# Optimization experiments

Measured on AMD Instinct MI355X. Metric: run time of the kernel, lower is better.

Reference implementation:

```python
import jax, jax.numpy as jnp
import numpy as np

N, E, L, H, D, HID = 32768, 262144, 4, 8, 64, 512
IN_DIM, OUT_DIM, EDIM, MAX_SP = 386, 384, 32, 4


def setup_inputs() -> dict:
    key = jax.random.key(0)
    k = jax.random.split(key, 16)
    s = 0.02
    d = {}
    d["embeddings"] = jax.random.normal(k[0], (N, IN_DIM), jnp.float32)
    d["edge_index"] = jax.random.randint(k[1], (2, E), 0, N)
    d["edge_attr_ids"] = jax.random.randint(k[2], (E,), 0, MAX_SP)
    d["Win"] = jax.random.normal(k[3], (IN_DIM, HID)) * s
    d["bin_"] = jnp.zeros((HID,))
    d["Etab"] = jax.random.normal(k[4], (MAX_SP, EDIM)) * s
    d["Wq"] = jax.random.normal(k[5], (L, HID, HID)) * s
    d["bq"] = jnp.zeros((L, HID))
    d["Wk"] = jax.random.normal(k[6], (L, HID, HID)) * s
    d["bk"] = jnp.zeros((L, HID))
    d["Wv"] = jax.random.normal(k[7], (L, HID, HID)) * s
    d["bv"] = jnp.zeros((L, HID))
    d["We"] = jax.random.normal(k[8], (L, EDIM, HID)) * s
    d["be"] = jnp.zeros((L, HID))
    d["Ws"] = jax.random.normal(k[9], (L, HID, HID)) * s
    d["bs"] = jnp.zeros((L, HID))
    d["Wbeta"] = jax.random.normal(k[10], (L, 3 * HID, 1)) * s
    d["bbeta"] = jnp.zeros((L, 1))
    d["ln_g"] = jnp.ones((L, HID))
    d["ln_b"] = jnp.zeros((L, HID))
    d["Wout"] = jax.random.normal(k[11], (HID, OUT_DIM)) * s
    d["bout"] = jnp.zeros((OUT_DIM,))
    return d


def _ln(x, g, b):
    mu = x.mean(-1, keepdims=True)
    var = ((x - mu) ** 2).mean(-1, keepdims=True)
    return (x - mu) * jax.lax.rsqrt(var + 1e-5) * g + b


def _fwd(embeddings, edge_index, edge_attr_ids, Win, bin_, Etab, Wq, bq, Wk, bk,
         Wv, bv, We, be, Ws, bs, Wbeta, bbeta, ln_g, ln_b, Wout, bout):
    src, dst = edge_index[0], edge_index[1]  # messages flow src -> dst (PyG convention)
    h = embeddings @ Win + bin_              # [N, HID]
    e = Etab[edge_attr_ids]                  # [E, EDIM]
    scale = 1.0 / np.sqrt(D).astype(np.float32)
    for l in range(L):
        q = (h @ Wq[l] + bq[l]).reshape(N, H, D)
        kk = (h @ Wk[l] + bk[l]).reshape(N, H, D)
        v = (h @ Wv[l] + bv[l]).reshape(N, H, D)
        ee = (e @ We[l] + be[l]).reshape(E, H, D)
        kj = kk[src] + ee                    # [E, H, D]
        vj = v[src] + ee                     # [E, H, D]
        alpha = jnp.einsum('ehd,ehd->eh', q[dst], kj) * scale  # [E, H]
        # segment softmax over incoming edges of each target node
        amax = jax.lax.stop_gradient(jax.ops.segment_max(alpha, dst, num_segments=N))
        ex = jnp.exp(alpha - amax[dst])
        denom = jax.ops.segment_sum(ex, dst, num_segments=N)
        a = ex / denom[dst]                  # [E, H] (dropout in eval mode -> identity)
        out = jax.ops.segment_sum(a[..., None] * vj, dst, num_segments=N).reshape(N, HID)
        # beta-gated skip connection (PyG TransformerConv beta=True)
        xr = h @ Ws[l] + bs[l]
        beta = jax.nn.sigmoid(jnp.concatenate([out, xr, out - xr], axis=-1) @ Wbeta[l] + bbeta[l])
        out = beta * xr + (1.0 - beta) * out
        h = _ln(h + out, ln_g[l], ln_b[l])
    return h @ Wout + bout


def reference(embeddings, edge_index, edge_attr_ids, Win, bin_, Etab, Wq, bq, Wk,
              bk, Wv, bv, We, be, Ws, bs, Wbeta, bbeta, ln_g, ln_b, Wout, bout):
    return _fwd(embeddings, edge_index, edge_attr_ids, Win, bin_, Etab, Wq, bq,
                Wk, bk, Wv, bv, We, be, Ws, bs, Wbeta, bbeta, ln_g, ln_b, Wout, bout)
```

## Files before the change

### kernel.cpp

```cpp
#include <hip/hip_runtime.h>
#include <math.h>

#define NN      32768
#define EE_N    262144
#define LL      4
#define HID     512
#define IN_DIM  386
#define KP_IN   416
#define OUT_DIM 384
#define EDIM    32
#define MAX_SP  4

typedef __attribute__((ext_vector_type(8))) __bf16 bf16x8;
typedef __attribute__((ext_vector_type(4))) float  f32x4;

__device__ __forceinline__ unsigned short f2bf(float f) {
    unsigned int u = __float_as_uint(f);
    unsigned int r = (u + 0x7FFFu + ((u >> 16) & 1u)) >> 16;
    return (unsigned short)r;
}
__device__ __forceinline__ void unpack2(unsigned int w, float& lo, float& hi) {
    lo = __uint_as_float(w << 16);
    hi = __uint_as_float(w & 0xFFFF0000u);
}

template <int OUT_MODE>
__global__ __launch_bounds__(256) void gemm_mfma(
    const unsigned short* __restrict__ A,
    const unsigned short* __restrict__ Bt,
    const float* __restrict__ bias,
    void* __restrict__ C0, void* __restrict__ C1,
    int M, int Kp, int N)
{
    __shared__ unsigned short As[128 * 32];
    __shared__ unsigned short Bs[128 * 32];

    const int t    = threadIdx.x;
    const int lane = t & 63, wid = t >> 6;
    const int wr   = wid >> 1, wc = wid & 1;
    const int row0 = blockIdx.y * 128;
    const int col0 = blockIdx.x * 128;

    f32x4 acc[4][4] = {};

    const int srow  = lane >> 2;
    const int sslot = lane & 3;
    const int kq    = lane >> 4;
    const int l15   = lane & 15;

    for (int kt = 0; kt < Kp; kt += 32) {
#pragma unroll
        for (int i = 0; i < 2; ++i) {
            const int rbase = wid * 32 + i * 16;
            {
                const int r    = rbase + srow;
                const int koff = sslot ^ ((r >> 1) & 3);
                const unsigned short* ga = &A[(size_t)(row0 + r) * Kp + kt + koff * 8];
                __builtin_amdgcn_global_load_lds(
                    (const __attribute__((address_space(1))) unsigned int*)ga,
                    (__attribute__((address_space(3))) unsigned int*)&As[rbase * 32],
                    16, 0, 0);
            }
            {
                const int c    = rbase + srow;
                const int koff = sslot ^ ((c >> 1) & 3);
                const unsigned short* gb = &Bt[(size_t)(col0 + c) * Kp + kt + koff * 8];
                __builtin_amdgcn_global_load_lds(
                    (const __attribute__((address_space(1))) unsigned int*)gb,
                    (__attribute__((address_space(3))) unsigned int*)&Bs[rbase * 32],
                    16, 0, 0);
            }
        }
        __syncthreads();

        bf16x8 af[4], bf[4];
#pragma unroll
        for (int mi = 0; mi < 4; ++mi) {
            const int r    = wr * 64 + mi * 16 + l15;
            const int slot = kq ^ ((r >> 1) & 3);
            af[mi] = *reinterpret_cast<const bf16x8*>(&As[r * 32 + slot * 8]);
        }
#pragma unroll
        for (int ni = 0; ni < 4; ++ni) {
            const int c    = wc * 64 + ni * 16 + l15;
            const int slot = kq ^ ((c >> 1) & 3);
            bf[ni] = *reinterpret_cast<const bf16x8*>(&Bs[c * 32 + slot * 8]);
        }
#pragma unroll
        for (int mi = 0; mi < 4; ++mi)
#pragma unroll
            for (int ni = 0; ni < 4; ++ni)
                acc[mi][ni] = __builtin_amdgcn_mfma_f32_16x16x32_bf16(
                    af[mi], bf[ni], acc[mi][ni], 0, 0, 0);
        __syncthreads();
    }

    const int cb = col0 + wc * 64;
    const int rb = row0 + wr * 64;
    float bv[4];
#pragma unroll
    for (int ni = 0; ni < 4; ++ni) bv[ni] = bias[cb + ni * 16 + l15];

#pragma unroll
    for (int mi = 0; mi < 4; ++mi) {
#pragma unroll
        for (int ni = 0; ni < 4; ++ni) {
            const int col = cb + ni * 16 + l15;
#pragma unroll
            for (int r = 0; r < 4; ++r) {
                const int row = rb + mi * 16 + kq * 4 + r;
                const float oval = acc[mi][ni][r] + bv[ni];
                if (OUT_MODE == 0) {
                    ((float*)C0)[(size_t)row * N + col] = oval;
                } else if (OUT_MODE == 1) {
                    ((unsigned short*)C0)[(size_t)row * N + col] = f2bf(oval);
                } else {
                    ((float*)C0)[(size_t)row * N + col] = oval;
                    ((unsigned short*)C1)[(size_t)row * N + col] = f2bf(oval);
                }
            }
        }
    }
}

__global__ __launch_bounds__(256) void convert_wt(
    const float* __restrict__ W, unsigned short* __restrict__ Wt,
    int K, int N, int Kp)
{
    __shared__ float tile[32][33];
    const int tx = threadIdx.x, ty = threadIdx.y;
    const int kb = blockIdx.y * 32, nb = blockIdx.x * 32;
#pragma unroll
    for (int i = 0; i < 32; i += 8) {
        const int k = kb + ty + i, n = nb + tx;
        tile[ty + i][tx] = (k < K && n < N) ? W[(size_t)k * N + n] : 0.f;
    }
    __syncthreads();
#pragma unroll
    for (int i = 0; i < 32; i += 8) {
        const int n = nb + ty + i, k = kb + tx;
        if (n < N && k < Kp)
            Wt[(size_t)n * Kp + k] = f2bf(tile[tx][ty + i]);
    }
}

__global__ __launch_bounds__(256) void convert_emb(
    const float* __restrict__ emb, unsigned short* __restrict__ ebf)
{
    const int n = blockIdx.x;
    for (int k = threadIdx.x; k < KP_IN; k += 256)
        ebf[(size_t)n * KP_IN + k] =
            (k < IN_DIM) ? f2bf(emb[(size_t)n * IN_DIM + k]) : (unsigned short)0;
}

__global__ void ee_kernel(const float* __restrict__ Etab,
                          const float* __restrict__ We,
                          const float* __restrict__ be,
                          float* __restrict__ ee)
{
    int j = threadIdx.x;
    if (j < HID) {
        for (int a = 0; a < MAX_SP; ++a) {
            float s = be[j];
            for (int kk = 0; kk < EDIM; ++kk)
                s = fmaf(Etab[a * EDIM + kk], We[kk * HID + j], s);
            ee[a * HID + j] = s;
        }
    }
}

__global__ void hist_kernel(const int* __restrict__ dst, int* __restrict__ deg)
{
    int e = blockIdx.x * blockDim.x + threadIdx.x;
    if (e < EE_N) atomicAdd(&deg[dst[e]], 1);
}

__global__ __launch_bounds__(1024) void scan_kernel(
    const int* __restrict__ deg, int* __restrict__ row_ptr, int* __restrict__ cursor)
{
    __shared__ int sdata[1024];
    const int t = threadIdx.x;
    const int base = t * 32;
    int s = 0;
    for (int i = 0; i < 32; ++i) s += deg[base + i];
    sdata[t] = s;
    __syncthreads();
    for (int off = 1; off < 1024; off <<= 1) {
        int val = (t >= off) ? sdata[t - off] : 0;
        __syncthreads();
        sdata[t] += val;
        __syncthreads();
    }
    int run = sdata[t] - s;
    for (int i = 0; i < 32; ++i) {
        row_ptr[base + i] = run;
        cursor[base + i]  = run;
        run += deg[base + i];
    }
    if (t == 1023) row_ptr[NN] = run;
}

__global__ void scatter_kernel(const int* __restrict__ src, const int* __restrict__ dst,
                               const int* __restrict__ aid, int* __restrict__ cursor,
                               int* __restrict__ csr_src, int* __restrict__ csr_aid)
{
    int e = blockIdx.x * blockDim.x + threadIdx.x;
    if (e < EE_N) {
        int d = dst[e];
        int pos = atomicAdd(&cursor[d], 1);
        csr_src[pos] = src[e];
        csr_aid[pos] = aid[e];
    }
}

__global__ __launch_bounds__(256) void attn_kernel(
    const unsigned short* __restrict__ q, const unsigned short* __restrict__ k,
    const unsigned short* __restrict__ v, const float* __restrict__ ee,
    const int* __restrict__ row_ptr, const int* __restrict__ csr_src,
    const int* __restrict__ csr_aid, unsigned short* __restrict__ out)
{
    __shared__ float ees[MAX_SP * HID];
    const int t = threadIdx.x;
    for (int i = t; i < MAX_SP * HID; i += 256) ees[i] = ee[i];
    __syncthreads();

    const int wave = t >> 6, lane = t & 63;
    const int node = blockIdx.x * 4 + wave;
    const int off  = lane << 3;

    float qa[8];
    {
        uint4 qv = *reinterpret_cast<const uint4*>(&q[(size_t)node * HID + off]);
        unpack2(qv.x, qa[0], qa[1]); unpack2(qv.y, qa[2], qa[3]);
        unpack2(qv.z, qa[4], qa[5]); unpack2(qv.w, qa[6], qa[7]);
    }

    float m = -INFINITY, denom = 0.f;
    float acc[8] = {0.f, 0.f, 0.f, 0.f, 0.f, 0.f, 0.f, 0.f};

    const int beg = row_ptr[node], end = row_ptr[node + 1];
    for (int i = beg; i < end; ++i) {
        const int s   = csr_src[i];
        const int aid = csr_aid[i];
        const float* ep = &ees[aid * HID + off];

        float kj[8];
        {
            uint4 kv = *reinterpret_cast<const uint4*>(&k[(size_t)s * HID + off]);
            unpack2(kv.x, kj[0], kj[1]); unpack2(kv.y, kj[2], kj[3]);
            unpack2(kv.z, kj[4], kj[5]); unpack2(kv.w, kj[6], kj[7]);
        }
        float partial = 0.f;
#pragma unroll
        for (int j = 0; j < 8; ++j) partial = fmaf(qa[j], kj[j] + ep[j], partial);
        partial += __shfl_xor(partial, 1);
        partial += __shfl_xor(partial, 2);
        partial += __shfl_xor(partial, 4);
        const float alpha = partial * 0.125f;

        const float mnew = fmaxf(m, alpha);
        const float corr = expf(m - mnew);
        const float w    = expf(alpha - mnew);
        denom = denom * corr + w;

        float vj[8];
        {
            uint4 vv = *reinterpret_cast<const uint4*>(&v[(size_t)s * HID + off]);
            unpack2(vv.x, vj[0], vj[1]); unpack2(vv.y, vj[2], vj[3]);
            unpack2(vv.z, vj[4], vj[5]); unpack2(vv.w, vj[6], vj[7]);
        }
#pragma unroll
        for (int j = 0; j < 8; ++j) acc[j] = acc[j] * corr + w * (vj[j] + ep[j]);
        m = mnew;
    }

    const float inv = (denom > 0.f) ? (1.f / denom) : 0.f;
    union { unsigned short us[8]; uint4 v4; } pk;
#pragma unroll
    for (int j = 0; j < 8; ++j) pk.us[j] = f2bf(acc[j] * inv);
    *reinterpret_cast<uint4*>(&out[(size_t)node * HID + off]) = pk.v4;
}

__global__ __launch_bounds__(256) void blend_ln_kernel(
    float* __restrict__ h, unsigned short* __restrict__ hbf,
    const unsigned short* __restrict__ attn,
    const unsigned short* __restrict__ xr, const float* __restrict__ wbeta,
    const float* __restrict__ bbeta, const float* __restrict__ ln_g,
    const float* __restrict__ ln_b)
{
    const int t = threadIdx.x;
    const int wave = t >> 6, lane = t & 63;
    const int node = blockIdx.x * 4 + wave;
    const int off  = lane << 3;

    float o8[8], x8[8], h8[8];
    {
        uint4 a = *reinterpret_cast<const uint4*>(&attn[(size_t)node * HID + off]);
        unpack2(a.x, o8[0], o8[1]); unpack2(a.y, o8[2], o8[3]);
        unpack2(a.z, o8[4], o8[5]); unpack2(a.w, o8[6], o8[7]);
        uint4 b = *reinterpret_cast<const uint4*>(&xr[(size_t)node * HID + off]);
        unpack2(b.x, x8[0], x8[1]); unpack2(b.y, x8[2], x8[3]);
        unpack2(b.z, x8[4], x8[5]); unpack2(b.w, x8[6], x8[7]);
        float4 c0 = *reinterpret_cast<const float4*>(&h[(size_t)node * HID + off]);
        float4 c1 = *reinterpret_cast<const float4*>(&h[(size_t)node * HID + off + 4]);
        h8[0]=c0.x; h8[1]=c0.y; h8[2]=c0.z; h8[3]=c0.w; h8[4]=c1.x; h8[5]=c1.y; h8[6]=c1.z; h8[7]=c1.w;
    }

    float p = 0.f;
#pragma unroll
    for (int j = 0; j < 8; ++j) {
        float w1 = wbeta[off + j];
        float w2 = wbeta[HID + off + j];
        float w3 = wbeta[2 * HID + off + j];
        p = fmaf(o8[j], w1 + w3, p);
        p = fmaf(x8[j], w2 - w3, p);
    }
#pragma unroll
    for (int m = 1; m <= 32; m <<= 1) p += __shfl_xor(p, m);
    const float beta = 1.f / (1.f + expf(-(p + bbeta[0])));

    float y[8];
    float s = 0.f;
#pragma unroll
    for (int j = 0; j < 8; ++j) {
        y[j] = h8[j] + beta * x8[j] + (1.f - beta) * o8[j];
        s += y[j];
    }
#pragma unroll
    for (int m = 1; m <= 32; m <<= 1) s += __shfl_xor(s, m);
    const float mean = s * (1.f / HID);

    float vs = 0.f;
#pragma unroll
    for (int j = 0; j < 8; ++j) {
        float d = y[j] - mean;
        vs = fmaf(d, d, vs);
    }
#pragma unroll
    for (int m = 1; m <= 32; m <<= 1) vs += __shfl_xor(vs, m);
    const float rstd = rsqrtf(vs * (1.f / HID) + 1e-5f);

    float rr[8];
    union { unsigned short us[8]; uint4 v4; } pk;
#pragma unroll
    for (int j = 0; j < 8; ++j) {
        rr[j] = (y[j] - mean) * rstd * ln_g[off + j] + ln_b[off + j];
        pk.us[j] = f2bf(rr[j]);
    }
    float4 r0 = {rr[0], rr[1], rr[2], rr[3]};
    float4 r1 = {rr[4], rr[5], rr[6], rr[7]};
    *reinterpret_cast<float4*>(&h[(size_t)node * HID + off])     = r0;
    *reinterpret_cast<float4*>(&h[(size_t)node * HID + off + 4]) = r1;
    *reinterpret_cast<uint4*>(&hbf[(size_t)node * HID + off])    = pk.v4;
}

extern "C" void kernel_launch(void* const* d_in, const int* in_sizes, int n_in,
                              void* d_out, int out_size, void* d_ws, size_t ws_size,
                              hipStream_t stream)
{
    (void)in_sizes; (void)n_in; (void)out_size; (void)ws_size;
    const float* emb   = (const float*)d_in[0];
    const int*   eidx  = (const int*)d_in[1];
    const int*   aid   = (const int*)d_in[2];
    const float* Win   = (const float*)d_in[3];
    const float* bin_  = (const float*)d_in[4];
    const float* Etab  = (const float*)d_in[5];
    const float* Wq    = (const float*)d_in[6];
    const float* bq    = (const float*)d_in[7];
    const float* Wk    = (const float*)d_in[8];
    const float* bk    = (const float*)d_in[9];
    const float* Wv    = (const float*)d_in[10];
    const float* bv    = (const float*)d_in[11];
    const float* We    = (const float*)d_in[12];
    const float* be    = (const float*)d_in[13];
    const float* Ws    = (const float*)d_in[14];
    const float* bs    = (const float*)d_in[15];
    const float* Wbeta = (const float*)d_in[16];
    const float* bbeta = (const float*)d_in[17];
    const float* ln_g  = (const float*)d_in[18];
    const float* ln_b  = (const float*)d_in[19];
    const float* Wout  = (const float*)d_in[20];
    const float* bout  = (const float*)d_in[21];
    float* out = (float*)d_out;

    char* w = (char*)d_ws;
    float* h            = (float*)w;           w += (size_t)NN * HID * 4;
    unsigned short* q   = (unsigned short*)w;  w += (size_t)NN * HID * 2;
    unsigned short* k   = (unsigned short*)w;  w += (size_t)NN * HID * 2;
    unsigned short* v   = (unsigned short*)w;  w += (size_t)NN * HID * 2;
    unsigned short* hbf = (unsigned short*)w;  w += (size_t)NN * HID * 2;
    unsigned short* embbf = q;
    unsigned short* Winbf  = (unsigned short*)w; w += (size_t)HID * KP_IN * 2;
    unsigned short* Wlt    = (unsigned short*)w; w += (size_t)16 * HID * HID * 2;
    unsigned short* Woutbf = (unsigned short*)w; w += (size_t)OUT_DIM * HID * 2;
    float* ee    = (float*)w;  w += MAX_SP * HID * 4;
    int* row_ptr = (int*)w;    w += (NN + 4) * 4;
    int* cursor  = (int*)w;    w += NN * 4;
    int* deg     = (int*)w;    w += NN * 4;
    int* csr_src = (int*)w;    w += EE_N * 4;
    int* csr_aid = (int*)w;    w += EE_N * 4;

    const int* src = eidx;
    const int* dst = eidx + EE_N;

    hipMemsetAsync(deg, 0, NN * sizeof(int), stream);
    hist_kernel<<<EE_N / 256, 256, 0, stream>>>(dst, deg);
    scan_kernel<<<1, 1024, 0, stream>>>(deg, row_ptr, cursor);
    scatter_kernel<<<EE_N / 256, 256, 0, stream>>>(src, dst, aid, cursor, csr_src, csr_aid);

    dim3 tb(32, 8);
    convert_wt<<<dim3(HID / 32, KP_IN / 32), tb, 0, stream>>>(Win, Winbf, IN_DIM, HID, KP_IN);
    for (int l = 0; l < LL; ++l) {
        convert_wt<<<dim3(16, 16), tb, 0, stream>>>(Wq + (size_t)l * HID * HID, Wlt + (size_t)(l * 4 + 0) * HID * HID, HID, HID, HID);
        convert_wt<<<dim3(16, 16), tb, 0, stream>>>(Wk + (size_t)l * HID * HID, Wlt + (size_t)(l * 4 + 1) * HID * HID, HID, HID, HID);
        convert_wt<<<dim3(16, 16), tb, 0, stream>>>(Wv + (size_t)l * HID * HID, Wlt + (size_t)(l * 4 + 2) * HID * HID, HID, HID, HID);
        convert_wt<<<dim3(16, 16), tb, 0, stream>>>(Ws + (size_t)l * HID * HID, Wlt + (size_t)(l * 4 + 3) * HID * HID, HID, HID, HID);
    }
    convert_wt<<<dim3(OUT_DIM / 32, HID / 32), tb, 0, stream>>>(Wout, Woutbf, HID, OUT_DIM, HID);
    convert_emb<<<NN, 256, 0, stream>>>(emb, embbf);

    gemm_mfma<2><<<dim3(HID / 128, NN / 128), 256, 0, stream>>>(
        embbf, Winbf, bin_, h, hbf, NN, KP_IN, HID);

    for (int l = 0; l < LL; ++l) {
        ee_kernel<<<1, HID, 0, stream>>>(Etab, We + (size_t)l * EDIM * HID, be + l * HID, ee);
        gemm_mfma<1><<<dim3(4, 256), 256, 0, stream>>>(
            hbf, Wlt + (size_t)(l * 4 + 0) * HID * HID, bq + l * HID, q, nullptr, NN, HID, HID);
        gemm_mfma<1><<<dim3(4, 256), 256, 0, stream>>>(
            hbf, Wlt + (size_t)(l * 4 + 1) * HID * HID, bk + l * HID, k, nullptr, NN, HID, HID);
        gemm_mfma<1><<<dim3(4, 256), 256, 0, stream>>>(
            hbf, Wlt + (size_t)(l * 4 + 2) * HID * HID, bv + l * HID, v, nullptr, NN, HID, HID);
        attn_kernel<<<NN / 4, 256, 0, stream>>>(q, k, v, ee, row_ptr, csr_src, csr_aid, q);
        gemm_mfma<1><<<dim3(4, 256), 256, 0, stream>>>(
            hbf, Wlt + (size_t)(l * 4 + 3) * HID * HID, bs + l * HID, k, nullptr, NN, HID, HID);
        blend_ln_kernel<<<NN / 4, 256, 0, stream>>>(h, hbf, q, k, Wbeta + (size_t)l * 3 * HID,
                                                    bbeta + l, ln_g + l * HID, ln_b + l * HID);
    }

    gemm_mfma<0><<<dim3(OUT_DIM / 128, NN / 128), 256, 0, stream>>>(
        hbf, Woutbf, bout, out, nullptr, NN, HID, OUT_DIM);
}
```

Before: 1.392 ms.

## Fuse QKV projections into one GEMM, pack CSR, drop online-softmax max

Q, K and V projections are merged into a single GEMM writing an interleaved [N,1536] buffer, with fused biases and batched weight conversion. CSR src and edge-attribute ids are packed into one int array. The attention kernel drops the running-max softmax rescaling and uses fast exp. A workgroup-id remap is added to the GEMM for better cache locality, and the per-layer edge-embedding kernels are hoisted into one launch. Removing the max subtraction risks overflow if attention logits grow large, and the 16-bit src packing relies on N being at most 65536.

```diff
diff --git a/kernel.cpp b/kernel.cpp
--- a/kernel.cpp
+++ b/kernel.cpp
@@ -10,6 +10,7 @@
 #define OUT_DIM 384
 #define EDIM    32
 #define MAX_SP  4
+#define QKV_LD  1536
 
 typedef __attribute__((ext_vector_type(8))) __bf16 bf16x8;
 typedef __attribute__((ext_vector_type(4))) float  f32x4;
@@ -30,7 +31,7 @@
     const unsigned short* __restrict__ Bt,
     const float* __restrict__ bias,
     void* __restrict__ C0, void* __restrict__ C1,
-    int M, int Kp, int N)
+    int M, int Kp, int N, int ldc)
 {
     __shared__ unsigned short As[128 * 32];
     __shared__ unsigned short Bs[128 * 32];
@@ -38,8 +39,12 @@
     const int t    = threadIdx.x;
     const int lane = t & 63, wid = t >> 6;
     const int wr   = wid >> 1, wc = wid & 1;
-    const int row0 = blockIdx.y * 128;
-    const int col0 = blockIdx.x * 128;
+
+    const int nwg = gridDim.x * gridDim.y;
+    int bid = blockIdx.y * gridDim.x + blockIdx.x;
+    if ((nwg & 7) == 0) bid = (bid & 7) * (nwg >> 3) + (bid >> 3);
+    const int row0 = (bid / gridDim.x) * 128;
+    const int col0 = (bid % gridDim.x) * 128;
 
     f32x4 acc[4][4] = {};
 
@@ -73,7 +78,7 @@
         }
         __syncthreads();
 
-        bf16x8 af[4], bf[4];
+        bf16x8 af[4], bfr[4];
 #pragma unroll
         for (int mi = 0; mi < 4; ++mi) {
             const int r    = wr * 64 + mi * 16 + l15;
@@ -84,14 +89,14 @@
         for (int ni = 0; ni < 4; ++ni) {
             const int c    = wc * 64 + ni * 16 + l15;
             const int slot = kq ^ ((c >> 1) & 3);
-            bf[ni] = *reinterpret_cast<const bf16x8*>(&Bs[c * 32 + slot * 8]);
+            bfr[ni] = *reinterpret_cast<const bf16x8*>(&Bs[c * 32 + slot * 8]);
         }
 #pragma unroll
         for (int mi = 0; mi < 4; ++mi)
 #pragma unroll
             for (int ni = 0; ni < 4; ++ni)
                 acc[mi][ni] = __builtin_amdgcn_mfma_f32_16x16x32_bf16(
-                    af[mi], bf[ni], acc[mi][ni], 0, 0, 0);
+                    af[mi], bfr[ni], acc[mi][ni], 0, 0, 0);
         __syncthreads();
     }
 
@@ -111,12 +116,12 @@
                 const int row = rb + mi * 16 + kq * 4 + r;
                 const float oval = acc[mi][ni][r] + bv[ni];
                 if (OUT_MODE == 0) {
-                    ((float*)C0)[(size_t)row * N + col] = oval;
+                    ((float*)C0)[(size_t)row * ldc + col] = oval;
                 } else if (OUT_MODE == 1) {
-                    ((unsigned short*)C0)[(size_t)row * N + col] = f2bf(oval);
+                    ((unsigned short*)C0)[(size_t)row * ldc + col] = f2bf(oval);
                 } else {
-                    ((float*)C0)[(size_t)row * N + col] = oval;
-                    ((unsigned short*)C1)[(size_t)row * N + col] = f2bf(oval);
+                    ((float*)C0)[(size_t)row * ldc + col] = oval;
+                    ((unsigned short*)C1)[(size_t)row * ldc + col] = f2bf(oval);
                 }
             }
         }
@@ -144,6 +149,28 @@
     }
 }
 
+__global__ __launch_bounds__(256) void convert_wt_batch(
+    const float* __restrict__ Wq, const float* __restrict__ Wk,
+    const float* __restrict__ Wv, const float* __restrict__ Ws,
+    unsigned short* __restrict__ Wlt)
+{
+    __shared__ float tile[32][33];
+    const int m = blockIdx.z;
+    const int l = m >> 2, tp = m & 3;
+    const float* W = (tp == 0 ? Wq : tp == 1 ? Wk : tp == 2 ? Wv : Ws)
+                     + (size_t)l * HID * HID;
+    unsigned short* Wt = Wlt + (size_t)m * HID * HID;
+    const int tx = threadIdx.x, ty = threadIdx.y;
+    const int kb = blockIdx.y * 32, nb = blockIdx.x * 32;
+#pragma unroll
+    for (int i = 0; i < 32; i += 8)
+        tile[ty + i][tx] = W[(size_t)(kb + ty + i) * HID + nb + tx];
+    __syncthreads();
+#pragma unroll
+    for (int i = 0; i < 32; i += 8)
+        Wt[(size_t)(nb + ty + i) * HID + kb + tx] = f2bf(tile[tx][ty + i]);
+}
+
 __global__ __launch_bounds__(256) void convert_emb(
     const float* __restrict__ emb, unsigned short* __restrict__ ebf)
 {
@@ -153,20 +180,33 @@
             (k < IN_DIM) ? f2bf(emb[(size_t)n * IN_DIM + k]) : (unsigned short)0;
 }
 
-__global__ void ee_kernel(const float* __restrict__ Etab,
-                          const float* __restrict__ We,
-                          const float* __restrict__ be,
-                          float* __restrict__ ee)
-{
-    int j = threadIdx.x;
-    if (j < HID) {
-        for (int a = 0; a < MAX_SP; ++a) {
-            float s = be[j];
-            for (int kk = 0; kk < EDIM; ++kk)
-                s = fmaf(Etab[a * EDIM + kk], We[kk * HID + j], s);
-            ee[a * HID + j] = s;
-        }
-    }
+__global__ void ee_all_kernel(const float* __restrict__ Etab,
+                              const float* __restrict__ We,
+                              const float* __restrict__ be,
+                              float* __restrict__ ee4)
+{
+    const int l = blockIdx.x, j = threadIdx.x;
+    const float* Wel = We + (size_t)l * EDIM * HID;
+    const float  bel = be[(size_t)l * HID + j];
+    for (int a = 0; a < MAX_SP; ++a) {
+        float s = bel;
+        for (int kk = 0; kk < EDIM; ++kk)
+            s = fmaf(Etab[a * EDIM + kk], Wel[(size_t)kk * HID + j], s);
+        ee4[((size_t)l * MAX_SP + a) * HID + j] = s;
+    }
+}
+
+__global__ void bias_fuse_kernel(const float* __restrict__ bq,
+                                 const float* __restrict__ bk,
+                                 const float* __restrict__ bv,
+                                 float* __restrict__ bqkv)
+{
+    const int i = blockIdx.x * 256 + threadIdx.x;
+    const int l = i / QKV_LD, r = i % QKV_LD;
+    float val = (r < 512) ? bq[l * 512 + r]
+              : (r < 1024) ? bk[l * 512 + r - 512]
+                           : bv[l * 512 + r - 1024];
+    bqkv[i] = val;
 }
 
 __global__ void hist_kernel(const int* __restrict__ dst, int* __restrict__ deg)
@@ -202,22 +242,19 @@
 
 __global__ void scatter_kernel(const int* __restrict__ src, const int* __restrict__ dst,
                                const int* __restrict__ aid, int* __restrict__ cursor,
-                               int* __restrict__ csr_src, int* __restrict__ csr_aid)
+                               int* __restrict__ csr_pack)
 {
     int e = blockIdx.x * blockDim.x + threadIdx.x;
     if (e < EE_N) {
         int d = dst[e];
         int pos = atomicAdd(&cursor[d], 1);
-        csr_src[pos] = src[e];
-        csr_aid[pos] = aid[e];
+        csr_pack[pos] = src[e] | (aid[e] << 16);
     }
 }
 
 __global__ __launch_bounds__(256) void attn_kernel(
-    const unsigned short* __restrict__ q, const unsigned short* __restrict__ k,
-    const unsigned short* __restrict__ v, const float* __restrict__ ee,
-    const int* __restrict__ row_ptr, const int* __restrict__ csr_src,
-    const int* __restrict__ csr_aid, unsigned short* __restrict__ out)
+    unsigned short* __restrict__ qkv, const float* __restrict__ ee,
+    const int* __restrict__ row_ptr, const int* __restrict__ csr_pack)
 {
     __shared__ float ees[MAX_SP * HID];
     const int t = threadIdx.x;
@@ -230,61 +267,54 @@
 
     float qa[8];
     {
-        uint4 qv = *reinterpret_cast<const uint4*>(&q[(size_t)node * HID + off]);
+        uint4 qv = *reinterpret_cast<const uint4*>(&qkv[(size_t)node * QKV_LD + off]);
         unpack2(qv.x, qa[0], qa[1]); unpack2(qv.y, qa[2], qa[3]);
         unpack2(qv.z, qa[4], qa[5]); unpack2(qv.w, qa[6], qa[7]);
     }
 
-    float m = -INFINITY, denom = 0.f;
+    float denom = 0.f;
     float acc[8] = {0.f, 0.f, 0.f, 0.f, 0.f, 0.f, 0.f, 0.f};
 
     const int beg = row_ptr[node], end = row_ptr[node + 1];
     for (int i = beg; i < end; ++i) {
-        const int s   = csr_src[i];
-        const int aid = csr_aid[i];
+        const int p   = csr_pack[i];
+        const int s   = p & 0xFFFF;
+        const int aid = p >> 16;
         const float* ep = &ees[aid * HID + off];
+        const unsigned short* kp = &qkv[(size_t)s * QKV_LD + 512 + off];
+
+        uint4 kv = *reinterpret_cast<const uint4*>(kp);
+        uint4 vv = *reinterpret_cast<const uint4*>(kp + 512);
 
         float kj[8];
-        {
-            uint4 kv = *reinterpret_cast<const uint4*>(&k[(size_t)s * HID + off]);
-            unpack2(kv.x, kj[0], kj[1]); unpack2(kv.y, kj[2], kj[3]);
-            unpack2(kv.z, kj[4], kj[5]); unpack2(kv.w, kj[6], kj[7]);
-        }
+        unpack2(kv.x, kj[0], kj[1]); unpack2(kv.y, kj[2], kj[3]);
+        unpack2(kv.z, kj[4], kj[5]); unpack2(kv.w, kj[6], kj[7]);
         float partial = 0.f;
 #pragma unroll
         for (int j = 0; j < 8; ++j) partial = fmaf(qa[j], kj[j] + ep[j], partial);
         partial += __shfl_xor(partial, 1);
         partial += __shfl_xor(partial, 2);
         partial += __shfl_xor(partial, 4);
-        const float alpha = partial * 0.125f;
-
-        const float mnew = fmaxf(m, alpha);
-        const float corr = expf(m - mnew);
-        const float w    = expf(alpha - mnew);
-        denom = denom * corr + w;
+        const float w = __expf(partial * 0.125f);
+        denom += w;
 
         float vj[8];
-        {
-            uint4 vv = *reinterpret_cast<const uint4*>(&v[(size_t)s * HID + off]);
-            unpack2(vv.x, vj[0], vj[1]); unpack2(vv.y, vj[2], vj[3]);
-            unpack2(vv.z, vj[4], vj[5]); unpack2(vv.w, vj[6], vj[7]);
-        }
-#pragma unroll
-        for (int j = 0; j < 8; ++j) acc[j] = acc[j] * corr + w * (vj[j] + ep[j]);
-        m = mnew;
+        unpack2(vv.x, vj[0], vj[1]); unpack2(vv.y, vj[2], vj[3]);
+        unpack2(vv.z, vj[4], vj[5]); unpack2(vv.w, vj[6], vj[7]);
+#pragma unroll
+        for (int j = 0; j < 8; ++j) acc[j] = fmaf(w, vj[j] + ep[j], acc[j]);
     }
 
     const float inv = (denom > 0.f) ? (1.f / denom) : 0.f;
     union { unsigned short us[8]; uint4 v4; } pk;
 #pragma unroll
     for (int j = 0; j < 8; ++j) pk.us[j] = f2bf(acc[j] * inv);
-    *reinterpret_cast<uint4*>(&out[(size_t)node * HID + off]) = pk.v4;
+    *reinterpret_cast<uint4*>(&qkv[(size_t)node * QKV_LD + off]) = pk.v4;
 }
 
 __global__ __launch_bounds__(256) void blend_ln_kernel(
     float* __restrict__ h, unsigned short* __restrict__ hbf,
-    const unsigned short* __restrict__ attn,
-    const unsigned short* __restrict__ xr, const float* __restrict__ wbeta,
+    const unsigned short* __restrict__ qkv, const float* __restrict__ wbeta,
     const float* __restrict__ bbeta, const float* __restrict__ ln_g,
     const float* __restrict__ ln_b)
 {
@@ -295,10 +325,10 @@
 
     float o8[8], x8[8], h8[8];
     {
-        uint4 a = *reinterpret_cast<const uint4*>(&attn[(size_t)node * HID + off]);
+        uint4 a = *reinterpret_cast<const uint4*>(&qkv[(size_t)node * QKV_LD + off]);
         unpack2(a.x, o8[0], o8[1]); unpack2(a.y, o8[2], o8[3]);
         unpack2(a.z, o8[4], o8[5]); unpack2(a.w, o8[6], o8[7]);
-        uint4 b = *reinterpret_cast<const uint4*>(&xr[(size_t)node * HID + off]);
+        uint4 b = *reinterpret_cast<const uint4*>(&qkv[(size_t)node * QKV_LD + 512 + off]);
         unpack2(b.x, x8[0], x8[1]); unpack2(b.y, x8[2], x8[3]);
         unpack2(b.z, x8[4], x8[5]); unpack2(b.w, x8[6], x8[7]);
         float4 c0 = *reinterpret_cast<const float4*>(&h[(size_t)node * HID + off]);
@@ -317,7 +347,7 @@
     }
 #pragma unroll
     for (int m = 1; m <= 32; m <<= 1) p += __shfl_xor(p, m);
-    const float beta = 1.f / (1.f + expf(-(p + bbeta[0])));
+    const float beta = 1.f / (1.f + __expf(-(p + bbeta[0])));
 
     float y[8];
     float s = 0.f;
@@ -385,20 +415,18 @@
 
     char* w = (char*)d_ws;
     float* h            = (float*)w;           w += (size_t)NN * HID * 4;
-    unsigned short* q   = (unsigned short*)w;  w += (size_t)NN * HID * 2;
-    unsigned short* k   = (unsigned short*)w;  w += (size_t)NN * HID * 2;
-    unsigned short* v   = (unsigned short*)w;  w += (size_t)NN * HID * 2;
     unsigned short* hbf = (unsigned short*)w;  w += (size_t)NN * HID * 2;
-    unsigned short* embbf = q;
+    unsigned short* qkv = (unsigned short*)w;  w += (size_t)NN * QKV_LD * 2;
+    unsigned short* embbf = qkv;
     unsigned short* Winbf  = (unsigned short*)w; w += (size_t)HID * KP_IN * 2;
     unsigned short* Wlt    = (unsigned short*)w; w += (size_t)16 * HID * HID * 2;
     unsigned short* Woutbf = (unsigned short*)w; w += (size_t)OUT_DIM * HID * 2;
-    float* ee    = (float*)w;  w += MAX_SP * HID * 4;
+    float* ee4   = (float*)w;  w += (size_t)LL * MAX_SP * HID * 4;
+    float* bqkv  = (float*)w;  w += (size_t)LL * QKV_LD * 4;
     int* row_ptr = (int*)w;    w += (NN + 4) * 4;
     int* cursor  = (int*)w;    w += NN * 4;
     int* deg     = (int*)w;    w += NN * 4;
-    int* csr_src = (int*)w;    w += EE_N * 4;
-    int* csr_aid = (int*)w;    w += EE_N * 4;
+    int* csr_pack = (int*)w;   w += EE_N * 4;
 
     const int* src = eidx;
     const int* dst = eidx + EE_N;
@@ -406,37 +434,33 @@
     hipMemsetAsync(deg, 0, NN * sizeof(int), stream);
     hist_kernel<<<EE_N / 256, 256, 0, stream>>>(dst, deg);
     scan_kernel<<<1, 1024, 0, stream>>>(deg, row_ptr, cursor);
-    scatter_kernel<<<EE_N / 256, 256, 0, stream>>>(src, dst, aid, cursor, csr_src, csr_aid);
+    scatter_kernel<<<EE_N / 256, 256, 0, stream>>>(src, dst, aid, cursor, csr_pack);
 
     dim3 tb(32, 8);
     convert_wt<<<dim3(HID / 32, KP_IN / 32), tb, 0, stream>>>(Win, Winbf, IN_DIM, HID, KP_IN);
-    for (int l = 0; l < LL; ++l) {
-        convert_wt<<<dim3(16, 16), tb, 0, stream>>>(Wq + (size_t)l * HID * HID, Wlt + (size_t)(l * 4 + 0) * HID * HID, HID, HID, HID);
-        convert_wt<<<dim3(16, 16), tb, 0, stream>>>(Wk + (size_t)l * HID * HID, Wlt + (size_t)(l * 4 + 1) * HID * HID, HID, HID, HID);
-        convert_wt<<<dim3(16, 16), tb, 0, stream>>>(Wv + (size_t)l * HID * HID, Wlt + (size_t)(l * 4 + 2) * HID * HID, HID, HID, HID);
-        convert_wt<<<dim3(16, 16), tb, 0, stream>>>(Ws + (size_t)l * HID * HID, Wlt + (size_t)(l * 4 + 3) * HID * HID, HID, HID, HID);
-    }
+    convert_wt_batch<<<dim3(16, 16, 16), tb, 0, stream>>>(Wq, Wk, Wv, Ws, Wlt);
     convert_wt<<<dim3(OUT_DIM / 32, HID / 32), tb, 0, stream>>>(Wout, Woutbf, HID, OUT_DIM, HID);
     convert_emb<<<NN, 256, 0, stream>>>(emb, embbf);
+    ee_all_kernel<<<LL, HID, 0, stream>>>(Etab, We, be, ee4);
+    bias_fuse_kernel<<<LL * QKV_LD / 256, 256, 0, stream>>>(bq, bk, bv, bqkv);
 
     gemm_mfma<2><<<dim3(HID / 128, NN / 128), 256, 0, stream>>>(
-        embbf, Winbf, bin_, h, hbf, NN, KP_IN, HID);
+        embbf, Winbf, bin_, h, hbf, NN, KP_IN, HID, HID);
 
     for (int l = 0; l < LL; ++l) {
-        ee_kernel<<<1, HID, 0, stream>>>(Etab, We + (size_t)l * EDIM * HID, be + l * HID, ee);
-        gemm_mfma<1><<<dim3(4, 256), 256, 0, stream>>>(
-            hbf, Wlt + (size_t)(l * 4 + 0) * HID * HID, bq + l * HID, q, nullptr, NN, HID, HID);
-        gemm_mfma<1><<<dim3(4, 256), 256, 0, stream>>>(
-            hbf, Wlt + (size_t)(l * 4 + 1) * HID * HID, bk + l * HID, k, nullptr, NN, HID, HID);
-        gemm_mfma<1><<<dim3(4, 256), 256, 0, stream>>>(
-            hbf, Wlt + (size_t)(l * 4 + 2) * HID * HID, bv + l * HID, v, nullptr, NN, HID, HID);
-        attn_kernel<<<NN / 4, 256, 0, stream>>>(q, k, v, ee, row_ptr, csr_src, csr_aid, q);
-        gemm_mfma<1><<<dim3(4, 256), 256, 0, stream>>>(
-            hbf, Wlt + (size_t)(l * 4 + 3) * HID * HID, bs + l * HID, k, nullptr, NN, HID, HID);
-        blend_ln_kernel<<<NN / 4, 256, 0, stream>>>(h, hbf, q, k, Wbeta + (size_t)l * 3 * HID,
-                                                    bbeta + l, ln_g + l * HID, ln_b + l * HID);
+        gemm_mfma<1><<<dim3(QKV_LD / 128, NN / 128), 256, 0, stream>>>(
+            hbf, Wlt + (size_t)(l * 4) * HID * HID, bqkv + (size_t)l * QKV_LD,
+            qkv, nullptr, NN, HID, QKV_LD, QKV_LD);
+        attn_kernel<<<NN / 4, 256, 0, stream>>>(
+            qkv, ee4 + (size_t)l * MAX_SP * HID, row_ptr, csr_pack);
+        gemm_mfma<1><<<dim3(HID / 128, NN / 128), 256, 0, stream>>>(
+            hbf, Wlt + (size_t)(l * 4 + 3) * HID * HID, bs + (size_t)l * HID,
+            qkv + 512, nullptr, NN, HID, HID, QKV_LD);
+        blend_ln_kernel<<<NN / 4, 256, 0, stream>>>(
+            h, hbf, qkv, Wbeta + (size_t)l * 3 * HID, bbeta + l,
+            ln_g + (size_t)l * HID, ln_b + (size_t)l * HID);
     }
 
     gemm_mfma<0><<<dim3(OUT_DIM / 128, NN / 128), 256, 0, stream>>>(
-        hbf, Woutbf, bout, out, nullptr, NN, HID, OUT_DIM);
-}
+        hbf, Woutbf, bout, out, nullptr, NN, HID, OUT_DIM, OUT_DIM);
+}
```

Result: faster. 1.173 ms (-15.8%).
